# Performance work log

Measured on AMD Instinct MI355X. Metric: run time of the kernel, lower is better.

Reference implementation:

```python
import jax, jax.numpy as jnp
import numpy as np

# ---- config (matches init_kwargs) ----
NUM_HEADS = 8
HEAD_DIM = 48
IN_CH = 384
OUT_CH = 384
AGENTS_HW = (7, 7)
CLUSTERS_HW = (2, 2)
NUM_MODULES = 2          # ['PartitionalClustering', 'FuzzyClustering']
N_GROUPS = 1 + 2 * NUM_MODULES   # p + (k, v) per module
D = NUM_HEADS * HEAD_DIM          # 384
NUM_CLUSTERS = CLUSTERS_HW[0] * CLUSTERS_HW[1]   # 4 per module
NUM_ALL_CLUSTERS = NUM_MODULES * NUM_CLUSTERS    # 8
EPS = 1e-6


def adaptive_avg_pool(x, oh, ow):
    # x: [b, c, H, W], H % oh == 0, W % ow == 0 -> exact block mean
    b, c, H, W = x.shape
    return x.reshape(b, c, oh, H // oh, ow, W // ow).mean(axis=(3, 5))


def setup_inputs() -> dict:
    key = jax.random.key(0)
    ks = jax.random.split(key, 6)
    B, H, W = 16, 56, 56
    x = jax.random.normal(ks[0], (B, IN_CH, H, W), dtype=jnp.float32)
    # proj: 1x1 linear in_channels -> N_GROUPS * D
    proj_w = jax.random.normal(ks[1], (N_GROUPS * D, IN_CH), dtype=jnp.float32) * (IN_CH ** -0.5)
    proj_b = jnp.zeros((N_GROUPS * D,), dtype=jnp.float32)
    sim_alpha = jnp.ones((NUM_ALL_CLUSTERS,), dtype=jnp.float32)
    sim_beta = jnp.zeros((NUM_ALL_CLUSTERS,), dtype=jnp.float32)
    proj2_w = jax.random.normal(ks[2], (OUT_CH, D), dtype=jnp.float32) * (D ** -0.5)
    proj2_b = jnp.zeros((OUT_CH,), dtype=jnp.float32)
    return {"x": x, "proj_w": proj_w, "proj_b": proj_b,
            "sim_alpha": sim_alpha, "sim_beta": sim_beta,
            "proj2_w": proj2_w, "proj2_b": proj2_b}


def _cluster_attention(i, k, v, kc, vc):
    # k: [b, c, Na] agent keys; v: [b, Na, c] agent values
    # kc, vc: [b, M, c] cluster centroids (keys / values)
    c = k.shape[1]
    scores = jnp.einsum('bmc,bcn->bmn', kc, k) / jnp.sqrt(jnp.float32(c))  # [b, M, Na]
    if i == 0:  # PartitionalClustering: attend over tokens per centroid
        attn = jax.nn.softmax(scores, axis=-1)
        agg = jnp.einsum('bmn,bnc->bmc', attn, v)
    else:       # FuzzyClustering: soft membership over clusters, normalized average
        memb = jax.nn.softmax(scores, axis=1)                              # over clusters
        agg = jnp.einsum('bmn,bnc->bmc', memb, v) / (memb.sum(axis=-1, keepdims=True) + EPS)
    return agg + vc  # with_cluster_bias=True


def reference(x, proj_w, proj_b, sim_alpha, sim_beta, proj2_w, proj2_b):
    B, C, H, W = x.shape
    # proj (1x1 linear over channels)
    y = jnp.einsum('bchw,oc->bohw', x, proj_w) + proj_b[None, :, None, None]
    y = y.reshape(B, N_GROUPS, D, H, W).transpose(1, 0, 2, 3, 4)
    b = B * NUM_HEADS
    c = HEAD_DIM
    y = y.reshape(N_GROUPS, b, c, H, W)
    p, r = y[0], y[1:]
    r = r.reshape(NUM_MODULES, 2, b, c, H, W)

    ah, aw = AGENTS_HW
    na = ah * aw
    agg_list = []
    for i in range(NUM_MODULES):  # fixed small structural loop
        k_full, v_full = r[i, 0], r[i, 1]
        kc = adaptive_avg_pool(k_full, *CLUSTERS_HW).reshape(b, c, NUM_CLUSTERS).transpose(0, 2, 1)
        vc = adaptive_avg_pool(v_full, *CLUSTERS_HW).reshape(b, c, NUM_CLUSTERS).transpose(0, 2, 1)
        k = adaptive_avg_pool(k_full, ah, aw).reshape(b, c, na)             # [b, c, Na]
        v = adaptive_avg_pool(v_full, ah, aw).reshape(b, c, na).transpose(0, 2, 1)  # [b, Na, c]
        agg_list.append(_cluster_attention(i, k, v, kc, vc))
    agg = jnp.concatenate(agg_list, axis=1)  # [b, M_all, c]

    p_agents = adaptive_avg_pool(p, ah, aw).reshape(b, c, na)  # [b, c, Na]
    # cosine similarity between centroid aggregates and query tokens
    agg_n = agg / (jnp.linalg.norm(agg, axis=-1, keepdims=True) + EPS)
    p_n = p_agents / (jnp.linalg.norm(p_agents, axis=1, keepdims=True) + EPS)
    sim = jnp.einsum('bmc,bcn->bmn', agg_n, p_n)  # [b, M_all, Na]
    similarity = sim_alpha[None, :, None] * sim + sim_beta[None, :, None]
    assignment = jax.nn.softmax(similarity, axis=1)  # over clusters

    out = jnp.einsum('bmc,bmn->bcn', agg, assignment)  # [b, c, Na]
    out = out.reshape(b, c, ah, aw)
    # bilinear upsample (half-pixel centers == torch align_corners=False)
    out = jax.image.resize(out, (b, c, H, W), method='linear')
    out = out.reshape(B, D, H, W)
    out = jnp.einsum('bdhw,od->bohw', out, proj2_w) + proj2_b[None, :, None, None]
    return out
```

## Files before the change

### kernel.cpp

```cpp
#include <hip/hip_runtime.h>
#include <math.h>

#define CIN    384
#define NPIX   3136
#define P_PAD  896
#define ZPSTR  319488

typedef float vf4 __attribute__((ext_vector_type(4)));
typedef __attribute__((ext_vector_type(4))) float f32x4;
typedef __attribute__((ext_vector_type(8))) short bf16x8;
typedef __attribute__((ext_vector_type(8))) unsigned short u16x8;

__device__ __forceinline__ unsigned short f2bf(float f) {
    unsigned u = __float_as_uint(f);
    u = (u + 0x7FFF + ((u >> 16) & 1)) >> 16;
    return (unsigned short)u;
}
__device__ __forceinline__ float bf2f(unsigned short h) {
    return __uint_as_float(((unsigned)h) << 16);
}

__global__ __launch_bounds__(256) void k_front(const float* __restrict__ x,
                                               const float* __restrict__ W,
                                               unsigned short* __restrict__ Xhi,
                                               unsigned short* __restrict__ Xlo,
                                               unsigned short* __restrict__ Whi,
                                               unsigned short* __restrict__ Wlo) {
    int blk = blockIdx.x;
    int t = threadIdx.x;
    if (blk >= 6144) {
        int i = (blk - 6144) * 256 + t;
        float w = W[i];
        unsigned short hi = f2bf(w);
        Whi[i] = hi;
        Wlo[i] = f2bf(w - bf2f(hi));
        return;
    }
    int Bi = blk / CIN;
    int ch = blk - Bi * CIN;
    __shared__ float ps[56][14];
    __shared__ float s14[14][14];
    const float* xp = x + (size_t)(Bi * CIN + ch) * NPIX;
    for (int p = t; p < 784; p += 256) {
        int row = p / 14, cb = p % 14;
        const vf4 v = __builtin_nontemporal_load(
            reinterpret_cast<const vf4*>(xp + row * 56 + cb * 4));
        ps[row][cb] = v.x + v.y + v.z + v.w;
    }
    __syncthreads();
    if (t < 196) {
        int ri = t / 14, cb = t % 14;
        s14[ri][cb] = ps[4*ri][cb] + ps[4*ri+1][cb] + ps[4*ri+2][cb] + ps[4*ri+3][cb];
    }
    __syncthreads();
    if (t < 49) {
        int i = t / 7, j = t % 7;
        float s = (s14[2*i][2*j] + s14[2*i][2*j+1] + s14[2*i+1][2*j] + s14[2*i+1][2*j+1])
                  * (1.0f / 64.0f);
        int p = Bi * 49 + t;
        unsigned short hi = f2bf(s);
        Xhi[(size_t)p * 384 + ch] = hi;
        Xlo[(size_t)p * 384 + ch] = f2bf(s - bf2f(hi));
    } else if (t >= 64 && t < 68) {
        int m = t - 64;
        int mi = m / 2, mj = m % 2;
        float s = 0.f;
        for (int ri = 7*mi; ri < 7*mi + 7; ++ri)
            for (int cb = 7*mj; cb < 7*mj + 7; ++cb)
                s += s14[ri][cb];
        s *= (1.0f / 784.0f);
        int p = 784 + Bi * 4 + m;
        unsigned short hi = f2bf(s);
        Xhi[(size_t)p * 384 + ch] = hi;
        Xlo[(size_t)p * 384 + ch] = f2bf(s - bf2f(hi));
    }
}

__global__ __launch_bounds__(512) void k_fuse(
        const unsigned short* __restrict__ Whi, const unsigned short* __restrict__ Wlo,
        const unsigned short* __restrict__ Xhi, const unsigned short* __restrict__ Xlo,
        const float* __restrict__ proj_b,
        const float* __restrict__ alpha, const float* __restrict__ beta,
        float* __restrict__ osmall) {
    int bb = blockIdx.x;
    int Bi = bb >> 3, head = bb & 7;
    __shared__ float yT[16560];
    __shared__ float e0[4][49], memb[4][49];
    __shared__ float rowmax0[4], esum0[4], msum[4];
    __shared__ float agg[8][48];
    __shared__ float anorm[8], pnorm[49];
    __shared__ float simL[8][49];
    __shared__ float assignW[8][49];
    unsigned short* sAh = (unsigned short*)yT;
    unsigned short* sAl = sAh + 9600;
    unsigned short* sBh = sAl + 9600;
    unsigned short* sBl = sBh + 2560;
    int t = threadIdx.x;
    int lane = t & 63, w = t >> 6;
    int fr = lane & 15, fq = lane >> 4;

    f32x4 acc[2][4] = {};
    for (int k0 = 0; k0 < 384; k0 += 32) {
        for (int c = t; c < 960; c += 512) {
            int row = c >> 2, ko = (c & 3) * 8;
            int g = row / 48, cc = row - g * 48;
            size_t goff = (size_t)(g * 384 + head * 48 + cc) * 384 + k0 + ko;
            *(u16x8*)&sAh[row * 40 + ko] = *(const u16x8*)(Whi + goff);
            *(u16x8*)&sAl[row * 40 + ko] = *(const u16x8*)(Wlo + goff);
        }
        if (t < 212) {
            int row = t >> 2, ko = (t & 3) * 8;
            int p = row < 49 ? Bi * 49 + row : 784 + Bi * 4 + (row - 49);
            size_t goff = (size_t)p * 384 + k0 + ko;
            *(u16x8*)&sBh[row * 40 + ko] = *(const u16x8*)(Xhi + goff);
            *(u16x8*)&sBl[row * 40 + ko] = *(const u16x8*)(Xlo + goff);
        }
        __syncthreads();
        bf16x8 bh[4], bl[4];
#pragma unroll
        for (int nt = 0; nt < 4; ++nt) {
            int r = nt * 16 + fr;
            bh[nt] = *(const bf16x8*)&sBh[r * 40 + fq * 8];
            bl[nt] = *(const bf16x8*)&sBl[r * 40 + fq * 8];
        }
#pragma unroll
        for (int mi = 0; mi < 2; ++mi) {
            int mt = 2 * w + mi;
            if (mt < 15) {
                int r = mt * 16 + fr;
                bf16x8 ah = *(const bf16x8*)&sAh[r * 40 + fq * 8];
                bf16x8 al = *(const bf16x8*)&sAl[r * 40 + fq * 8];
#pragma unroll
                for (int nt = 0; nt < 4; ++nt) {
                    acc[mi][nt] = __builtin_amdgcn_mfma_f32_16x16x32_bf16(ah, bh[nt], acc[mi][nt], 0, 0, 0);
                    acc[mi][nt] = __builtin_amdgcn_mfma_f32_16x16x32_bf16(ah, bl[nt], acc[mi][nt], 0, 0, 0);
                    acc[mi][nt] = __builtin_amdgcn_mfma_f32_16x16x32_bf16(al, bh[nt], acc[mi][nt], 0, 0, 0);
                }
            }
        }
        __syncthreads();
    }
#pragma unroll
    for (int mi = 0; mi < 2; ++mi) {
        int mt = 2 * w + mi;
        if (mt < 15) {
#pragma unroll
            for (int j = 0; j < 4; ++j) {
                int m = mt * 16 + fq * 4 + j;
                int g = m / 48, cc = m - g * 48;
                float bb = proj_b[g * 384 + head * 48 + cc];
#pragma unroll
                for (int nt = 0; nt < 4; ++nt)
                    yT[m * 69 + nt * 16 + fr] = acc[mi][nt][j] + bb;
            }
        }
    }
    __syncthreads();

    const float scale = 0.14433756729740643f;
    if (t < 392) {
        int i = t / 196, r = t % 196;
        int m = r / 49, n = r % 49;
        int rbase = 48 + 96 * i;
        float s = 0.f;
        for (int cc = 0; cc < 48; ++cc)
            s += yT[(rbase + cc) * 69 + 49 + m] * yT[(rbase + cc) * 69 + n];
        s *= scale;
        if (i == 0) e0[m][n] = s; else memb[m][n] = s;
    }
    __syncthreads();
    if (t < 4) {
        float mx = -1e30f;
        for (int n = 0; n < 49; ++n) mx = fmaxf(mx, e0[t][n]);
        rowmax0[t] = mx;
    }
    __syncthreads();
    if (t < 196) { int m = t / 49, n = t % 49; e0[m][n] = expf(e0[m][n] - rowmax0[m]); }
    __syncthreads();
    if (t < 4) { float s = 0.f; for (int n = 0; n < 49; ++n) s += e0[t][n]; esum0[t] = s; }
    if (t >= 64 && t < 113) {
        int n = t - 64;
        float a0 = memb[0][n], a1 = memb[1][n], a2 = memb[2][n], a3 = memb[3][n];
        float mx = fmaxf(fmaxf(a0, a1), fmaxf(a2, a3));
        float x0 = expf(a0 - mx), x1 = expf(a1 - mx), x2 = expf(a2 - mx), x3 = expf(a3 - mx);
        float s = x0 + x1 + x2 + x3;
        memb[0][n] = x0 / s; memb[1][n] = x1 / s; memb[2][n] = x2 / s; memb[3][n] = x3 / s;
    }
    __syncthreads();
    if (t < 4) { float s = 0.f; for (int n = 0; n < 49; ++n) s += memb[t][n]; msum[t] = s; }
    __syncthreads();
    if (t < 384) {
        int row = t / 48, cc = t % 48;
        float a = 0.f;
        if (row < 4) {
            const float* vr = &yT[(96 + cc) * 69];
            for (int n = 0; n < 49; ++n) a += e0[row][n] * vr[n];
            agg[row][cc] = a / esum0[row] + vr[49 + row];
        } else {
            int m = row - 4;
            const float* vr = &yT[(192 + cc) * 69];
            for (int n = 0; n < 49; ++n) a += memb[m][n] * vr[n];
            agg[row][cc] = a / (msum[m] + 1e-6f) + vr[49 + m];
        }
    }
    __syncthreads();
    if (t < 8) {
        float s = 0.f;
        for (int cc = 0; cc < 48; ++cc) { float a = agg[t][cc]; s += a * a; }
        anorm[t] = sqrtf(s) + 1e-6f;
    }
    if (t >= 64 && t < 113) {
        int n = t - 64; float s = 0.f;
        for (int cc = 0; cc < 48; ++cc) { float a = yT[cc * 69 + n]; s += a * a; }
        pnorm[n] = sqrtf(s) + 1e-6f;
    }
    __syncthreads();
    if (t < 392) {
        int m = t / 49, n = t - m * 49;
        float dot = 0.f;
        for (int cc = 0; cc < 48; ++cc) dot += agg[m][cc] * yT[cc * 69 + n];
        simL[m][n] = alpha[m] * (dot / (anorm[m] * pnorm[n])) + beta[m];
    }
    __syncthreads();
    if (t < 49) {
        int n = t;
        float mx = -1e30f, e[8];
        for (int m = 0; m < 8; ++m) mx = fmaxf(mx, simL[m][n]);
        float ssum = 0.f;
        for (int m = 0; m < 8; ++m) { e[m] = expf(simL[m][n] - mx); ssum += e[m]; }
        float inv = 1.f / ssum;
        for (int m = 0; m < 8; ++m) assignW[m][n] = e[m] * inv;
    }
    __syncthreads();
    for (int idx = t; idx < 2352; idx += 512) {
        int cc = idx / 49, n = idx % 49;
        float s = 0.f;
        for (int m = 0; m < 8; ++m) s += agg[m][cc] * assignW[m][n];
        osmall[((size_t)Bi * 384 + head * 48 + cc) * 49 + n] = s;
    }
}

__global__ __launch_bounds__(256) void k_gemm2s(const float* __restrict__ osmall,
                                                const float* __restrict__ W2,
                                                float* __restrict__ zp) {
    int b = blockIdx.x;
    int kc = b & 3, ot = (b >> 2) % 24, Bi = b / 96;
    __shared__ float smem[1552 + 4992];
    int t = threadIdx.x;
    for (int idx = t; idx < 1536; idx += 256) {
        int r0 = idx / 96, c = idx - r0 * 96;
        smem[r0 * 97 + c] = W2[(size_t)(ot * 16 + r0) * 384 + kc * 96 + c];
    }
    const float4* src4 = reinterpret_cast<const float4*>(
        osmall + (size_t)(Bi * 384 + kc * 96) * 49);
    for (int idx = t; idx < 1176; idx += 256) {
        float4 f = src4[idx];
        int e = idx * 4;
        float vv[4] = {f.x, f.y, f.z, f.w};
#pragma unroll
        for (int j = 0; j < 4; ++j) {
            int ee = e + j;
            int kk2 = ee / 49, n2 = ee - kk2 * 49;
            smem[1552 + kk2 * 52 + n2] = vv[j];
        }
    }
    if (t < 96) {
        int o = 1552 + t * 52;
        smem[o + 49] = 0.f; smem[o + 50] = 0.f; smem[o + 51] = 0.f;
    }
    __syncthreads();

    float4 acc0 = {0,0,0,0}, acc1 = {0,0,0,0}, acc2 = {0,0,0,0}, acc3 = {0,0,0,0};
    int ks = 0, rgq = 0, nq = 0;
    if (t < 208) {
        ks = t / 52; int rem = t - ks * 52; rgq = rem / 13; nq = rem - rgq * 13;
        const float* WtB = smem + rgq * 4 * 97 + ks;
        const float* OsB = smem + 1552 + nq * 4 + ks * 52;
#pragma unroll
        for (int i = 0; i < 24; ++i) {
            float4 bb = *reinterpret_cast<const float4*>(OsB + i * 208);
            float a0 = WtB[i * 4];
            float a1 = WtB[97  + i * 4];
            float a2 = WtB[194 + i * 4];
            float a3 = WtB[291 + i * 4];
            acc0.x += a0 * bb.x; acc0.y += a0 * bb.y; acc0.z += a0 * bb.z; acc0.w += a0 * bb.w;
            acc1.x += a1 * bb.x; acc1.y += a1 * bb.y; acc1.z += a1 * bb.z; acc1.w += a1 * bb.w;
            acc2.x += a2 * bb.x; acc2.y += a2 * bb.y; acc2.z += a2 * bb.z; acc2.w += a2 * bb.w;
            acc3.x += a3 * bb.x; acc3.y += a3 * bb.y; acc3.z += a3 * bb.z; acc3.w += a3 * bb.w;
        }
    }
    __syncthreads();
    if (t < 208) {
        int base = ((ks * 16 + rgq * 4) * 13 + nq) * 4;
        *reinterpret_cast<float4*>(smem + 1552 + base)       = acc0;
        *reinterpret_cast<float4*>(smem + 1552 + base + 52)  = acc1;
        *reinterpret_cast<float4*>(smem + 1552 + base + 104) = acc2;
        *reinterpret_cast<float4*>(smem + 1552 + base + 156) = acc3;
    }
    __syncthreads();
    if (t < 208) {
        int r = t / 13, nq2 = t - r * 13;
        int o0 = (r * 13 + nq2) * 4;
        float4 s0 = *reinterpret_cast<const float4*>(smem + 1552 + o0);
        float4 s1 = *reinterpret_cast<const float4*>(smem + 1552 + o0 + 832);
        float4 s2 = *reinterpret_cast<const float4*>(smem + 1552 + o0 + 1664);
        float4 s3 = *reinterpret_cast<const float4*>(smem + 1552 + o0 + 2496);
        float4 s;
        s.x = s0.x + s1.x + s2.x + s3.x;
        s.y = s0.y + s1.y + s2.y + s3.y;
        s.z = s0.z + s1.z + s2.z + s3.z;
        s.w = s0.w + s1.w + s2.w + s3.w;
        *reinterpret_cast<float4*>(zp + (size_t)kc * ZPSTR +
            ((size_t)(Bi * 384 + ot * 16 + r)) * 52 + nq2 * 4) = s;
    }
}

__global__ __launch_bounds__(256) void k_up4(const float* __restrict__ zp,
                                             const float* __restrict__ b2,
                                             float* __restrict__ out) {
    int blk = blockIdx.x;
    int Bi = blk / 96, cg = blk - Bi * 96;
    int ch0 = cg * 4;
    __shared__ float zL[4][52];
    __shared__ float tmp[4][56][8];
    int t = threadIdx.x;
    if (t < 196) {
        int c = t / 49, n = t - c * 49;
        size_t base = (size_t)(Bi * 384 + ch0 + c) * 52 + n;
        zL[c][n] = zp[base] + zp[base + ZPSTR] + zp[base + 2 * (size_t)ZPSTR]
                 + zp[base + 3 * (size_t)ZPSTR] + b2[ch0 + c];
    }
    __syncthreads();
    for (int idx = t; idx < 1568; idx += 256) {
        int c = idx / 392, rem = idx - c * 392;
        int h = rem / 7, iw = rem - h * 7;
        float sh = (h - 3.5f) * 0.125f;
        int ih0; float fh;
        if (sh <= 0.f)      { ih0 = 0; fh = 0.f; }
        else if (sh >= 6.f) { ih0 = 6; fh = 0.f; }
        else                { ih0 = (int)sh; fh = sh - (float)ih0; }
        int ih1 = min(ih0 + 1, 6);
        float z0 = zL[c][ih0 * 7 + iw];
        tmp[c][h][iw] = z0 + fh * (zL[c][ih1 * 7 + iw] - z0);
    }
    __syncthreads();
    size_t obase = ((size_t)(Bi * 384 + ch0)) * (size_t)NPIX;
    for (int q = t; q < 3136; q += 256) {
        int c = q / 784, rem = q - c * 784;
        int h = rem / 14, qw = rem - h * 14;
        const float* tr = &tmp[c][h][0];
        vf4 o4;
#pragma unroll
        for (int j = 0; j < 4; ++j) {
            int w = qw * 4 + j;
            float sw = (w - 3.5f) * 0.125f;
            int iw0; float fw;
            if (sw <= 0.f)      { iw0 = 0; fw = 0.f; }
            else if (sw >= 6.f) { iw0 = 6; fw = 0.f; }
            else                { iw0 = (int)sw; fw = sw - (float)iw0; }
            int iw1 = min(iw0 + 1, 6);
            float t0 = tr[iw0];
            o4[j] = t0 + fw * (tr[iw1] - t0);
        }
        __builtin_nontemporal_store(o4,
            reinterpret_cast<vf4*>(out + obase + (size_t)q * 4));
    }
}

extern "C" void kernel_launch(void* const* d_in, const int* in_sizes, int n_in,
                              void* d_out, int out_size, void* d_ws, size_t ws_size,
                              hipStream_t stream) {
    const float* x      = (const float*)d_in[0];
    const float* proj_w = (const float*)d_in[1];
    const float* proj_b = (const float*)d_in[2];
    const float* alpha  = (const float*)d_in[3];
    const float* beta   = (const float*)d_in[4];
    const float* w2     = (const float*)d_in[5];
    const float* b2     = (const float*)d_in[6];
    float* out = (float*)d_out;
    float* ws  = (float*)d_ws;

    float* osmall = ws;
    unsigned short* Whi = (unsigned short*)(ws + (size_t)301056);
    unsigned short* Wlo = (unsigned short*)(ws + (size_t)669696);
    unsigned short* Xhi = (unsigned short*)(ws + (size_t)1038336);
    unsigned short* Xlo = (unsigned short*)(ws + (size_t)1210368);
    float* zp = ws + (size_t)1382400;

    k_front <<<dim3(9024), 256, 0, stream>>>(x, proj_w, Xhi, Xlo, Whi, Wlo);
    k_fuse  <<<dim3(128),  512, 0, stream>>>(Whi, Wlo, Xhi, Xlo, proj_b, alpha, beta, osmall);
    k_gemm2s<<<dim3(1536), 256, 0, stream>>>(osmall, w2, zp);
    k_up4   <<<dim3(1536), 256, 0, stream>>>(zp, b2, out);
}
```

Measured before the change: 78.83 us.

## Fuse second projection into upsample kernel and register-prefetch GEMM tiles in k_fuse

Removes the separate k_gemm2s kernel and its split-K partial buffer. The 384→384 projection of the 49 agent values is now computed inside the upsample kernel, reading a transposed osT layout written by k_fuse. k_fuse also prefetches the next K-slice of the bf16 hi/lo tiles into registers while the current slice runs its MFMAs, which overlaps global loads with compute. The cost is that each upsample block reloads all of osT for its batch (49x384 floats), repeated across its 96 blocks, and the projection itself runs as scalar FMA.

```diff
diff --git a/kernel.cpp b/kernel.cpp
--- a/kernel.cpp
+++ b/kernel.cpp
@@ -3,8 +3,6 @@
 
 #define CIN    384
 #define NPIX   3136
-#define P_PAD  896
-#define ZPSTR  319488
 
 typedef float vf4 __attribute__((ext_vector_type(4)));
 typedef __attribute__((ext_vector_type(4))) float f32x4;
@@ -81,7 +79,7 @@
         const unsigned short* __restrict__ Xhi, const unsigned short* __restrict__ Xlo,
         const float* __restrict__ proj_b,
         const float* __restrict__ alpha, const float* __restrict__ beta,
-        float* __restrict__ osmall) {
+        float* __restrict__ osT) {
     int bb = blockIdx.x;
     int Bi = bb >> 3, head = bb & 7;
     __shared__ float yT[16560];
@@ -99,23 +97,44 @@
     int lane = t & 63, w = t >> 6;
     int fr = lane & 15, fq = lane >> 4;
 
+    int row0 = t >> 2, ko0 = (t & 3) * 8;
+    int g0 = row0 / 48, cc0 = row0 - g0 * 48;
+    size_t aoff0 = (size_t)(g0 * 384 + head * 48 + cc0) * 384 + ko0;
+    int c1 = t + 512;
+    int row1 = c1 >> 2, ko1 = (c1 & 3) * 8;
+    int g1 = row1 / 48, cc1 = row1 - g1 * 48;
+    size_t aoff1 = (size_t)(g1 * 384 + head * 48 + cc1) * 384 + ko1;
+    int bko = (t & 3) * 8;
+    int brow = t >> 2;
+    int bp = brow < 49 ? Bi * 49 + brow : 784 + Bi * 4 + (brow - 49);
+    size_t boff = (size_t)bp * 384 + bko;
+
+    u16x8 rAh0, rAl0, rAh1, rAl1, rBh, rBl;
+    rAh0 = *(const u16x8*)(Whi + aoff0);
+    rAl0 = *(const u16x8*)(Wlo + aoff0);
+    if (t < 448) { rAh1 = *(const u16x8*)(Whi + aoff1); rAl1 = *(const u16x8*)(Wlo + aoff1); }
+    if (t < 212) { rBh  = *(const u16x8*)(Xhi + boff);  rBl  = *(const u16x8*)(Xlo + boff); }
+
     f32x4 acc[2][4] = {};
-    for (int k0 = 0; k0 < 384; k0 += 32) {
-        for (int c = t; c < 960; c += 512) {
-            int row = c >> 2, ko = (c & 3) * 8;
-            int g = row / 48, cc = row - g * 48;
-            size_t goff = (size_t)(g * 384 + head * 48 + cc) * 384 + k0 + ko;
-            *(u16x8*)&sAh[row * 40 + ko] = *(const u16x8*)(Whi + goff);
-            *(u16x8*)&sAl[row * 40 + ko] = *(const u16x8*)(Wlo + goff);
+    for (int step = 0; step < 12; ++step) {
+        *(u16x8*)&sAh[row0 * 40 + ko0] = rAh0;
+        *(u16x8*)&sAl[row0 * 40 + ko0] = rAl0;
+        if (t < 448) {
+            *(u16x8*)&sAh[row1 * 40 + ko1] = rAh1;
+            *(u16x8*)&sAl[row1 * 40 + ko1] = rAl1;
         }
         if (t < 212) {
-            int row = t >> 2, ko = (t & 3) * 8;
-            int p = row < 49 ? Bi * 49 + row : 784 + Bi * 4 + (row - 49);
-            size_t goff = (size_t)p * 384 + k0 + ko;
-            *(u16x8*)&sBh[row * 40 + ko] = *(const u16x8*)(Xhi + goff);
-            *(u16x8*)&sBl[row * 40 + ko] = *(const u16x8*)(Xlo + goff);
+            *(u16x8*)&sBh[brow * 40 + bko] = rBh;
+            *(u16x8*)&sBl[brow * 40 + bko] = rBl;
         }
         __syncthreads();
+        if (step < 11) {
+            int k0 = (step + 1) * 32;
+            rAh0 = *(const u16x8*)(Whi + aoff0 + k0);
+            rAl0 = *(const u16x8*)(Wlo + aoff0 + k0);
+            if (t < 448) { rAh1 = *(const u16x8*)(Whi + aoff1 + k0); rAl1 = *(const u16x8*)(Wlo + aoff1 + k0); }
+            if (t < 212) { rBh  = *(const u16x8*)(Xhi + boff + k0);  rBl  = *(const u16x8*)(Xlo + boff + k0); }
+        }
         bf16x8 bh[4], bl[4];
 #pragma unroll
         for (int nt = 0; nt < 4; ++nt) {
@@ -233,106 +252,54 @@
     }
     __syncthreads();
     for (int idx = t; idx < 2352; idx += 512) {
-        int cc = idx / 49, n = idx % 49;
+        int n = idx / 48, cc = idx - n * 48;
         float s = 0.f;
         for (int m = 0; m < 8; ++m) s += agg[m][cc] * assignW[m][n];
-        osmall[((size_t)Bi * 384 + head * 48 + cc) * 49 + n] = s;
-    }
-}
-
-__global__ __launch_bounds__(256) void k_gemm2s(const float* __restrict__ osmall,
-                                                const float* __restrict__ W2,
-                                                float* __restrict__ zp) {
-    int b = blockIdx.x;
-    int kc = b & 3, ot = (b >> 2) % 24, Bi = b / 96;
-    __shared__ float smem[1552 + 4992];
-    int t = threadIdx.x;
-    for (int idx = t; idx < 1536; idx += 256) {
-        int r0 = idx / 96, c = idx - r0 * 96;
-        smem[r0 * 97 + c] = W2[(size_t)(ot * 16 + r0) * 384 + kc * 96 + c];
-    }
-    const float4* src4 = reinterpret_cast<const float4*>(
-        osmall + (size_t)(Bi * 384 + kc * 96) * 49);
-    for (int idx = t; idx < 1176; idx += 256) {
-        float4 f = src4[idx];
-        int e = idx * 4;
-        float vv[4] = {f.x, f.y, f.z, f.w};
-#pragma unroll
-        for (int j = 0; j < 4; ++j) {
-            int ee = e + j;
-            int kk2 = ee / 49, n2 = ee - kk2 * 49;
-            smem[1552 + kk2 * 52 + n2] = vv[j];
-        }
-    }
-    if (t < 96) {
-        int o = 1552 + t * 52;
-        smem[o + 49] = 0.f; smem[o + 50] = 0.f; smem[o + 51] = 0.f;
-    }
-    __syncthreads();
-
-    float4 acc0 = {0,0,0,0}, acc1 = {0,0,0,0}, acc2 = {0,0,0,0}, acc3 = {0,0,0,0};
-    int ks = 0, rgq = 0, nq = 0;
-    if (t < 208) {
-        ks = t / 52; int rem = t - ks * 52; rgq = rem / 13; nq = rem - rgq * 13;
-        const float* WtB = smem + rgq * 4 * 97 + ks;
-        const float* OsB = smem + 1552 + nq * 4 + ks * 52;
-#pragma unroll
-        for (int i = 0; i < 24; ++i) {
-            float4 bb = *reinterpret_cast<const float4*>(OsB + i * 208);
-            float a0 = WtB[i * 4];
-            float a1 = WtB[97  + i * 4];
-            float a2 = WtB[194 + i * 4];
-            float a3 = WtB[291 + i * 4];
-            acc0.x += a0 * bb.x; acc0.y += a0 * bb.y; acc0.z += a0 * bb.z; acc0.w += a0 * bb.w;
-            acc1.x += a1 * bb.x; acc1.y += a1 * bb.y; acc1.z += a1 * bb.z; acc1.w += a1 * bb.w;
-            acc2.x += a2 * bb.x; acc2.y += a2 * bb.y; acc2.z += a2 * bb.z; acc2.w += a2 * bb.w;
-            acc3.x += a3 * bb.x; acc3.y += a3 * bb.y; acc3.z += a3 * bb.z; acc3.w += a3 * bb.w;
-        }
-    }
-    __syncthreads();
-    if (t < 208) {
-        int base = ((ks * 16 + rgq * 4) * 13 + nq) * 4;
-        *reinterpret_cast<float4*>(smem + 1552 + base)       = acc0;
-        *reinterpret_cast<float4*>(smem + 1552 + base + 52)  = acc1;
-        *reinterpret_cast<float4*>(smem + 1552 + base + 104) = acc2;
-        *reinterpret_cast<float4*>(smem + 1552 + base + 156) = acc3;
-    }
-    __syncthreads();
-    if (t < 208) {
-        int r = t / 13, nq2 = t - r * 13;
-        int o0 = (r * 13 + nq2) * 4;
-        float4 s0 = *reinterpret_cast<const float4*>(smem + 1552 + o0);
-        float4 s1 = *reinterpret_cast<const float4*>(smem + 1552 + o0 + 832);
-        float4 s2 = *reinterpret_cast<const float4*>(smem + 1552 + o0 + 1664);
-        float4 s3 = *reinterpret_cast<const float4*>(smem + 1552 + o0 + 2496);
-        float4 s;
-        s.x = s0.x + s1.x + s2.x + s3.x;
-        s.y = s0.y + s1.y + s2.y + s3.y;
-        s.z = s0.z + s1.z + s2.z + s3.z;
-        s.w = s0.w + s1.w + s2.w + s3.w;
-        *reinterpret_cast<float4*>(zp + (size_t)kc * ZPSTR +
-            ((size_t)(Bi * 384 + ot * 16 + r)) * 52 + nq2 * 4) = s;
-    }
-}
-
-__global__ __launch_bounds__(256) void k_up4(const float* __restrict__ zp,
+        osT[((size_t)(Bi * 49 + n)) * 384 + head * 48 + cc] = s;
+    }
+}
+
+__global__ __launch_bounds__(256) void k_upf(const float* __restrict__ osT,
+                                             const float* __restrict__ W2,
                                              const float* __restrict__ b2,
                                              float* __restrict__ out) {
     int blk = blockIdx.x;
     int Bi = blk / 96, cg = blk - Bi * 96;
     int ch0 = cg * 4;
+    __shared__ float W2L[4 * 388];
+    __shared__ float OsL[49 * 100];
     __shared__ float zL[4][52];
     __shared__ float tmp[4][56][8];
     int t = threadIdx.x;
-    if (t < 196) {
-        int c = t / 49, n = t - c * 49;
-        size_t base = (size_t)(Bi * 384 + ch0 + c) * 52 + n;
-        zL[c][n] = zp[base] + zp[base + ZPSTR] + zp[base + 2 * (size_t)ZPSTR]
-                 + zp[base + 3 * (size_t)ZPSTR] + b2[ch0 + c];
-    }
+    for (int i = t; i < 1536; i += 256)
+        W2L[(i / 384) * 388 + (i % 384)] = W2[(size_t)ch0 * 384 + i];
+    int c = t & 3, n = t >> 2;
+    float acc = 0.f;
+    for (int kc = 0; kc < 4; ++kc) {
+        __syncthreads();
+        for (int i = t; i < 49 * 24; i += 256) {
+            int nn = i / 24, j = i - nn * 24;
+            float4 f = *reinterpret_cast<const float4*>(
+                osT + ((size_t)(Bi * 49 + nn)) * 384 + kc * 96 + j * 4);
+            *reinterpret_cast<float4*>(&OsL[nn * 100 + j * 4]) = f;
+        }
+        __syncthreads();
+        if (t < 196) {
+            const float* wrow = W2L + c * 388 + kc * 96;
+            const float* orow = OsL + n * 100;
+#pragma unroll
+            for (int j = 0; j < 24; ++j) {
+                float4 wv = *reinterpret_cast<const float4*>(wrow + j * 4);
+                float4 ov = *reinterpret_cast<const float4*>(orow + j * 4);
+                acc += wv.x * ov.x + wv.y * ov.y + wv.z * ov.z + wv.w * ov.w;
+            }
+        }
+    }
+    __syncthreads();
+    if (t < 196) zL[c][n] = acc + b2[ch0 + c];
     __syncthreads();
     for (int idx = t; idx < 1568; idx += 256) {
-        int c = idx / 392, rem = idx - c * 392;
+        int cc = idx / 392, rem = idx - cc * 392;
         int h = rem / 7, iw = rem - h * 7;
         float sh = (h - 3.5f) * 0.125f;
         int ih0; float fh;
@@ -340,15 +307,15 @@
         else if (sh >= 6.f) { ih0 = 6; fh = 0.f; }
         else                { ih0 = (int)sh; fh = sh - (float)ih0; }
         int ih1 = min(ih0 + 1, 6);
-        float z0 = zL[c][ih0 * 7 + iw];
-        tmp[c][h][iw] = z0 + fh * (zL[c][ih1 * 7 + iw] - z0);
+        float z0 = zL[cc][ih0 * 7 + iw];
+        tmp[cc][h][iw] = z0 + fh * (zL[cc][ih1 * 7 + iw] - z0);
     }
     __syncthreads();
     size_t obase = ((size_t)(Bi * 384 + ch0)) * (size_t)NPIX;
     for (int q = t; q < 3136; q += 256) {
-        int c = q / 784, rem = q - c * 784;
+        int cc = q / 784, rem = q - cc * 784;
         int h = rem / 14, qw = rem - h * 14;
-        const float* tr = &tmp[c][h][0];
+        const float* tr = &tmp[cc][h][0];
         vf4 o4;
 #pragma unroll
         for (int j = 0; j < 4; ++j) {
@@ -380,15 +347,13 @@
     float* out = (float*)d_out;
     float* ws  = (float*)d_ws;
 
-    float* osmall = ws;
+    float* osT = ws;
     unsigned short* Whi = (unsigned short*)(ws + (size_t)301056);
     unsigned short* Wlo = (unsigned short*)(ws + (size_t)669696);
     unsigned short* Xhi = (unsigned short*)(ws + (size_t)1038336);
     unsigned short* Xlo = (unsigned short*)(ws + (size_t)1210368);
-    float* zp = ws + (size_t)1382400;
-
-    k_front <<<dim3(9024), 256, 0, stream>>>(x, proj_w, Xhi, Xlo, Whi, Wlo);
-    k_fuse  <<<dim3(128),  512, 0, stream>>>(Whi, Wlo, Xhi, Xlo, proj_b, alpha, beta, osmall);
-    k_gemm2s<<<dim3(1536), 256, 0, stream>>>(osmall, w2, zp);
-    k_up4   <<<dim3(1536), 256, 0, stream>>>(zp, b2, out);
-}
+
+    k_front<<<dim3(9024), 256, 0, stream>>>(x, proj_w, Xhi, Xlo, Whi, Wlo);
+    k_fuse <<<dim3(128),  512, 0, stream>>>(Whi, Wlo, Xhi, Xlo, proj_b, alpha, beta, osT);
+    k_upf  <<<dim3(1536), 256, 0, stream>>>(osT, w2, b2, out);
+}
```

New measurement: 81.17 us. +3.0%, slower.
